# Kernel optimization log

Hardware: AMD Instinct MI355X
Metric: run time of the kernel (lower is better)

The kernel has to match this reference:

```python
import jax, jax.numpy as jnp
import numpy as np

B, IN, OUT, K, RES, WDIM = 8, 512, 512, 3, 64, 512
CONV_RC = 1.0 / np.sqrt(K * K * IN).astype(np.float32)   # gain*lrmul/sqrt(fan_in), gain=lrmul=1
DENSE_RC = 1.0 / np.sqrt(WDIM).astype(np.float32)
CONV_INIT_STD = float(CONV_RC)   # init_std = he_std / lrmul
DENSE_INIT_STD = float(DENSE_RC)


def setup_inputs() -> dict:
    key = jax.random.key(0)
    k1, k2, k3, k4 = jax.random.split(key, 4)
    return {
        "x": jax.random.normal(k1, (B, IN, RES, RES), jnp.float32),
        "y": jax.random.normal(k2, (B, WDIM), jnp.float32),
        "w": jax.random.normal(k3, (K, K, IN, OUT), jnp.float32) * CONV_INIT_STD,
        "w_mod": jax.random.normal(k4, (WDIM, IN), jnp.float32) * DENSE_INIT_STD,
        "b_mod": jnp.zeros((IN,), jnp.float32),
    }


def reference(x, y, w, w_mod, b_mod):
    # equalized-lr runtime scaling
    w_s = w * CONV_RC                                   # [K,K,IN,OUT]
    # style: s = dense(y) + bias + 1
    s = y @ (w_mod * DENSE_RC) + b_mod + 1.0            # [B,IN]
    # modulate per-sample weights
    ww = w_s[None] * s[:, None, None, :, None]          # [B,K,K,IN,OUT]
    # demodulate
    d = jax.lax.rsqrt(jnp.sum(jnp.square(ww), axis=(1, 2, 3)) + 1e-8)  # [B,OUT]
    ww = ww * d[:, None, None, None, :]
    # fused modconv: grouped conv with groups = B
    xr = x.reshape(1, B * IN, RES, RES)
    wk = jnp.transpose(ww, (1, 2, 3, 0, 4)).reshape(K, K, IN, B * OUT)
    out = jax.lax.conv_general_dilated(
        xr, wk, window_strides=(1, 1), padding="SAME",
        dimension_numbers=("NCHW", "HWIO", "NCHW"),
        feature_group_count=B)
    return out.reshape(B, OUT, RES, RES)
```

## Files before the change

kernel.cpp:

```cpp
#include <hip/hip_runtime.h>
#include <hip/hip_bf16.h>

typedef __bf16 bf16x8 __attribute__((ext_vector_type(8)));
typedef float f32x16 __attribute__((ext_vector_type(16)));
typedef unsigned short u16;
typedef u16 u16x8 __attribute__((ext_vector_type(8)));

#define DENSE_RC 0.0441941738f
#define CONV_RC  0.0147313913f

__device__ inline u16 f2bf(float v) {
  union { float f; unsigned u; } x; x.f = v;
  unsigned r = x.u + 0x7fffu + ((x.u >> 16) & 1u);
  return (u16)(r >> 16);
}

__device__ inline void gload16(const void* g, void* l) {
  __builtin_amdgcn_global_load_lds(
      (const __attribute__((address_space(1))) unsigned int*)g,
      (__attribute__((address_space(3))) unsigned int*)l, 16, 0, 0);
}

__global__ void style_k(const float* __restrict__ y, const float* __restrict__ wm,
                        const float* __restrict__ bm, float* __restrict__ s) {
  const int tid = threadIdx.x, lane = tid & 63, wv = tid >> 6;
  const int idx = blockIdx.x * 64 + lane;
  const int b = idx >> 9, i = idx & 511;
  const float* yb = y + b * 512;
  float acc = 0.f;
  const int j0 = wv * 128;
#pragma unroll 8
  for (int j = j0; j < j0 + 128; ++j) acc += yb[j] * wm[j * 512 + i];
  __shared__ float red[4][64];
  red[wv][lane] = acc;
  __syncthreads();
  if (wv == 0) {
    float a = red[0][lane] + red[1][lane] + red[2][lane] + red[3][lane];
    s[idx] = a * DENSE_RC + bm[i] + 1.0f;
  }
}

__global__ void wsq_k(const float* __restrict__ w, float* __restrict__ wsq) {
  const int idx = blockIdx.x * 256 + threadIdx.x;
  float a = 0.f;
#pragma unroll
  for (int t = 0; t < 9; ++t) { float v = w[(size_t)t * 262144 + idx]; a += v * v; }
  wsq[idx] = a;
}

__global__ void demod_k(const float* __restrict__ s, const float* __restrict__ wsq,
                        float* __restrict__ dmd) {
  const int tid = threadIdx.x, lane = tid & 63, wv = tid >> 6;
  const int idx = blockIdx.x * 64 + lane;
  const int b = idx >> 9, o = idx & 511;
  const float* sb = s + b * 512;
  float a = 0.f;
  const int i0 = wv * 128;
#pragma unroll 4
  for (int i = i0; i < i0 + 128; ++i) { float sv = sb[i]; a += sv * sv * wsq[i * 512 + o]; }
  __shared__ float red[4][64];
  red[wv][lane] = a;
  __syncthreads();
  if (wv == 0) {
    float t = red[0][lane] + red[1][lane] + red[2][lane] + red[3][lane];
    dmd[idx] = rsqrtf(t * (CONV_RC * CONV_RC) + 1e-8f);
  }
}

__global__ void modw_k(const float* __restrict__ w, const float* __restrict__ s,
                       const float* __restrict__ dmd, u16* __restrict__ wwb) {
  const int blk = blockIdx.x;
  const int ob = blk & 7, ib = (blk >> 3) & 15, t = blk >> 7;
  __shared__ float lw[32][65];
  const int tid = threadIdx.x;
#pragma unroll
  for (int k = 0; k < 8; ++k) {
    const int e = tid + k * 256;
    const int i = e >> 6, o = e & 63;
    lw[i][o] = w[(size_t)t * 262144 + (size_t)(ib * 32 + i) * 512 + ob * 64 + o];
  }
  __syncthreads();
  const int oo = tid >> 2, q = tid & 3;
  const int ii0 = q * 8;
  for (int b = 0; b < 8; ++b) {
    const float f = CONV_RC * dmd[b * 512 + ob * 64 + oo];
    u16x8 pk;
#pragma unroll
    for (int j = 0; j < 8; ++j)
      pk[j] = f2bf(lw[ii0 + j][oo] * s[b * 512 + ib * 32 + ii0 + j] * f);
    *(u16x8*)(wwb + ((size_t)(b * 9 + t) * 512 + ob * 64 + oo) * 512 + ib * 32 + ii0) = pk;
  }
}

__global__ void border_k(u16* __restrict__ xpad) {
  const int idx = blockIdx.x * 256 + threadIdx.x;
  const int chunk = idx & 63;
  const int p = (idx >> 6) % 260;
  const int b = idx / (260 * 64);
  int row, col;
  if (p < 66)       { row = 0;       col = p; }
  else if (p < 132) { row = 65;      col = p - 66; }
  else if (p < 196) { row = p - 131; col = 0; }
  else              { row = p - 195; col = 65; }
  u16x8 z = {0, 0, 0, 0, 0, 0, 0, 0};
  *(u16x8*)(xpad + ((size_t)(b * 66 + row) * 66 + col) * 512 + chunk * 8) = z;
}

__global__ void fill_k(const float* __restrict__ x, u16* __restrict__ xpad) {
  const int blk = blockIdx.x;
  const int ib = blk & 3, hh = (blk >> 2) & 63, b = blk >> 8;
  __shared__ float lx[128][65];
  const int tid = threadIdx.x;
#pragma unroll
  for (int k = 0; k < 2; ++k) {
    const int u = tid + k * 256;
    const int i = u >> 2, w0 = (u & 3) * 16;
    const float* src = x + (size_t)((b * 512 + ib * 128 + i) * 64 + hh) * 64 + w0;
    float tmp[16];
    ((float4*)tmp)[0] = ((const float4*)src)[0];
    ((float4*)tmp)[1] = ((const float4*)src)[1];
    ((float4*)tmp)[2] = ((const float4*)src)[2];
    ((float4*)tmp)[3] = ((const float4*)src)[3];
#pragma unroll
    for (int j = 0; j < 16; ++j) lx[i][w0 + j] = tmp[j];
  }
  __syncthreads();
  const int c = tid >> 2, q = tid & 3;
  const size_t base = ((size_t)(b * 66 + hh + 1) * 66 + (c + 1)) * 512 + ib * 128;
#pragma unroll
  for (int k = 0; k < 4; ++k) {
    const int irow = k * 32 + q * 8;
    u16x8 pk;
#pragma unroll
    for (int j = 0; j < 8; ++j) pk[j] = f2bf(lx[irow + j][c]);
    *(u16x8*)(xpad + base + irow) = pk;
  }
}

__global__ __launch_bounds__(256, 2) void conv_k(const u16* __restrict__ xpad,
                                                 const u16* __restrict__ wwb,
                                                 float* __restrict__ out) {
  __shared__ __align__(1024) char SM[79104];
  const int raw = (int)blockIdx.x;
  const int pt = raw >> 6, ot = (raw >> 3) & 7, b = raw & 7;
  const int tid = threadIdx.x;
  const int lane = tid & 63, wv = tid >> 6;
  const int h0 = pt * 8;

  const size_t xbase = (size_t)(b * 66 + h0) * (66 * 512);

  const u16* sp[10];
#pragma unroll
  for (int r = 0; r < 10; ++r) {
    const int cc = tid + r * 256;
    if (cc < 1152) {
      const int lc = cc ^ ((cc >> 3) & 3);
      const int t = lc >> 7, o = (lc >> 1) & 63, i8 = lc & 1;
      sp[r] = wwb + ((size_t)(b * 9 + t) * 512 + ot * 64 + o) * 512 + i8 * 8;
    } else {
      const int p = cc - 1152;
      const int lc = p ^ ((p >> 3) & 3);
      const int rc = lc >> 1, i8 = lc & 1;
      sp[r] = xpad + xbase + (size_t)rc * 512 + i8 * 8;
    }
  }

  const int l2 = ((lane & 31) << 1) | (lane >> 5);
  const int AoffT = (l2 ^ ((l2 >> 3) & 3)) * 16;
  int Boff[4][3];
#pragma unroll
  for (int rr = 0; rr < 4; ++rr)
#pragma unroll
    for (int tx = 0; tx < 3; ++tx) {
      const int ch = ((2 * wv + rr) * 66 + tx) * 2 + l2;
      Boff[rr][tx] = (ch ^ ((ch >> 3) & 3)) * 16;
    }

  f32x16 acc[2][2][2];
#pragma unroll
  for (int mi = 0; mi < 2; ++mi)
#pragma unroll
    for (int hf = 0; hf < 2; ++hf)
#pragma unroll
      for (int n = 0; n < 2; ++n)
#pragma unroll
        for (int e = 0; e < 16; ++e) acc[mi][hf][n][e] = 0.f;

#define LOADB(bf, rr, tx, ofs) { \
    const char* _p = SM + (ofs) + 18432 + Boff[rr][tx]; \
    bf[0] = *(const bf16x8*)_p; bf[1] = *(const bf16x8*)(_p + 1024); }
#define LOADA(af, t, ofs) { \
    const char* _p = SM + (ofs) + AoffT + (t) * 2048; \
    af[0] = *(const bf16x8*)_p; af[1] = *(const bf16x8*)(_p + 1024); }
#define TAP(af, Blo, Bhi) \
    __builtin_amdgcn_s_setprio(1); \
    acc[0][0][0] = __builtin_amdgcn_mfma_f32_32x32x16_bf16(af[0], Blo[0], acc[0][0][0], 0, 0, 0); \
    acc[0][0][1] = __builtin_amdgcn_mfma_f32_32x32x16_bf16(af[0], Blo[1], acc[0][0][1], 0, 0, 0); \
    acc[0][1][0] = __builtin_amdgcn_mfma_f32_32x32x16_bf16(af[0], Bhi[0], acc[0][1][0], 0, 0, 0); \
    acc[0][1][1] = __builtin_amdgcn_mfma_f32_32x32x16_bf16(af[0], Bhi[1], acc[0][1][1], 0, 0, 0); \
    acc[1][0][0] = __builtin_amdgcn_mfma_f32_32x32x16_bf16(af[1], Blo[0], acc[1][0][0], 0, 0, 0); \
    acc[1][0][1] = __builtin_amdgcn_mfma_f32_32x32x16_bf16(af[1], Blo[1], acc[1][0][1], 0, 0, 0); \
    acc[1][1][0] = __builtin_amdgcn_mfma_f32_32x32x16_bf16(af[1], Bhi[0], acc[1][1][0], 0, 0, 0); \
    acc[1][1][1] = __builtin_amdgcn_mfma_f32_32x32x16_bf16(af[1], Bhi[1], acc[1][1][1], 0, 0, 0); \
    __builtin_amdgcn_s_setprio(0);

  auto stage = [&](int ofs) {
#pragma unroll
    for (int r = 0; r < 9; ++r)
      gload16(sp[r], SM + ofs + (tid + r * 256) * 16);
    if (tid < 168) gload16(sp[9], SM + ofs + (tid + 2304) * 16);
#pragma unroll
    for (int r = 0; r < 10; ++r) sp[r] += 16;
  };

  auto compute = [&](int ofs) {
#pragma unroll
    for (int tx = 0; tx < 3; ++tx) {
      bf16x8 R0[2], R1[2], R2[2], R3[2], af0[2], af1[2], af2[2];
      LOADB(R0, 0, tx, ofs);
      LOADB(R1, 1, tx, ofs);
      LOADA(af0, tx, ofs);
      TAP(af0, R0, R1);
      LOADB(R2, 2, tx, ofs);
      LOADA(af1, 3 + tx, ofs);
      TAP(af1, R1, R2);
      LOADB(R3, 3, tx, ofs);
      LOADA(af2, 6 + tx, ofs);
      TAP(af2, R2, R3);
    }
  };

  stage(0);
  asm volatile("s_waitcnt vmcnt(0)" ::: "memory");
  __syncthreads();

  int cofs = 0, nofs = 39552;
  for (int kb = 0; kb < 31; ++kb) {
    stage(nofs);
    compute(cofs);
    asm volatile("s_waitcnt vmcnt(0)" ::: "memory");
    __syncthreads();
    const int tsw = cofs; cofs = nofs; nofs = tsw;
  }
  compute(cofs);

  const int pxl = lane & 31, oh = (lane >> 5) * 4;
#pragma unroll
  for (int mi = 0; mi < 2; ++mi)
#pragma unroll
    for (int hf = 0; hf < 2; ++hf) {
      const int h = h0 + 2 * wv + hf;
#pragma unroll
      for (int n = 0; n < 2; ++n) {
        const int wc = n * 32 + pxl;
#pragma unroll
        for (int reg = 0; reg < 16; ++reg) {
          const int o = ot * 64 + mi * 32 + (reg & 3) + 8 * (reg >> 2) + oh;
          out[((size_t)(b * 512 + o) * 64 + h) * 64 + wc] = acc[mi][hf][n][reg];
        }
      }
    }
#undef LOADB
#undef LOADA
#undef TAP
}

extern "C" void kernel_launch(void* const* d_in, const int* in_sizes, int n_in,
                              void* d_out, int out_size, void* d_ws, size_t ws_size,
                              hipStream_t stream) {
  const float* x     = (const float*)d_in[0];
  const float* y     = (const float*)d_in[1];
  const float* w     = (const float*)d_in[2];
  const float* w_mod = (const float*)d_in[3];
  const float* b_mod = (const float*)d_in[4];
  float* out = (float*)d_out;

  char* ws = (char*)d_ws;
  float* s    = (float*)(ws);
  float* dmd  = (float*)(ws + 16384);
  float* wsq  = (float*)(ws + 32768);
  u16*   wwb  = (u16*)(ws + 32768 + 1048576);
  u16*   xpad = (u16*)(ws + 32768 + 1048576 + 37748736);

  style_k<<<64, 256, 0, stream>>>(y, w_mod, b_mod, s);
  wsq_k<<<1024, 256, 0, stream>>>(w, wsq);
  demod_k<<<64, 256, 0, stream>>>(s, wsq, dmd);
  modw_k<<<1152, 256, 0, stream>>>(w, s, dmd, wwb);
  border_k<<<520, 256, 0, stream>>>(xpad);
  fill_k<<<2048, 256, 0, stream>>>(x, xpad);
  conv_k<<<512, 256, 0, stream>>>(xpad, wwb, out);
}
```

Measured before the change: 185.9 us.

## Use single-buffered 32-channel K tiles instead of double-buffered 16-channel stages

The conv main loop now stages 32 input channels per iteration into one LDS buffer of about 79KB, replacing two ~40KB buffers of 16 channels. That halves the iteration count and the barriers. Each iteration now loads, waits, computes and syncs with no overlap of global loads against MFMA work, and the setprio hints are gone. The LDS layout and swizzle are rewritten to match the wider tiles, so each tap now issues twice as many MFMAs.

```diff
diff --git a/kernel.cpp b/kernel.cpp
--- a/kernel.cpp
+++ b/kernel.cpp
@@ -149,30 +149,34 @@
 
   const size_t xbase = (size_t)(b * 66 + h0) * (66 * 512);
 
-  const u16* sp[10];
-#pragma unroll
-  for (int r = 0; r < 10; ++r) {
+  const u16* aw[9];
+  const u16* ax[11];
+#pragma unroll
+  for (int r = 0; r < 9; ++r) {
     const int cc = tid + r * 256;
-    if (cc < 1152) {
-      const int lc = cc ^ ((cc >> 3) & 3);
-      const int t = lc >> 7, o = (lc >> 1) & 63, i8 = lc & 1;
-      sp[r] = wwb + ((size_t)(b * 9 + t) * 512 + ot * 64 + o) * 512 + i8 * 8;
-    } else {
-      const int p = cc - 1152;
-      const int lc = p ^ ((p >> 3) & 3);
-      const int rc = lc >> 1, i8 = lc & 1;
-      sp[r] = xpad + xbase + (size_t)rc * 512 + i8 * 8;
-    }
-  }
-
-  const int l2 = ((lane & 31) << 1) | (lane >> 5);
-  const int AoffT = (l2 ^ ((l2 >> 3) & 3)) * 16;
+    const int lc = cc ^ ((cc >> 3) & 3);
+    const int i8 = lc & 3, o = (lc >> 2) & 63, t = lc >> 8;
+    aw[r] = wwb + ((size_t)(b * 9 + t) * 512 + ot * 64 + o) * 512 + i8 * 8;
+  }
+#pragma unroll
+  for (int r = 0; r < 11; ++r) {
+    const int c2 = tid + r * 256;
+    const int lc = c2 ^ ((c2 >> 3) & 3);
+    const int i8 = lc & 3, rc = lc >> 2;
+    ax[r] = xpad + xbase + (size_t)rc * 512 + i8 * 8;
+  }
+  const bool extra = (tid < 80);
+
+  const int pxl = lane & 31, i5 = lane >> 5;
+  const int cbA = pxl * 4 + i5;
+  const int AbO = (cbA ^ ((cbA >> 3) & 3)) * 16;
   int Boff[4][3];
 #pragma unroll
   for (int rr = 0; rr < 4; ++rr)
 #pragma unroll
     for (int tx = 0; tx < 3; ++tx) {
-      const int ch = ((2 * wv + rr) * 66 + tx) * 2 + l2;
+      const int m = (2 * wv + rr) * 66 + tx + pxl;
+      const int ch = m * 4 + i5;
       Boff[rr][tx] = (ch ^ ((ch >> 3) & 3)) * 16;
     }
 
@@ -186,65 +190,69 @@
 #pragma unroll
         for (int e = 0; e < 16; ++e) acc[mi][hf][n][e] = 0.f;
 
-#define LOADB(bf, rr, tx, ofs) { \
-    const char* _p = SM + (ofs) + 18432 + Boff[rr][tx]; \
-    bf[0] = *(const bf16x8*)_p; bf[1] = *(const bf16x8*)(_p + 1024); }
-#define LOADA(af, t, ofs) { \
-    const char* _p = SM + (ofs) + AoffT + (t) * 2048; \
-    af[0] = *(const bf16x8*)_p; af[1] = *(const bf16x8*)(_p + 1024); }
+#define LOADB(R, rr, tx) { \
+    const int _o = Boff[rr][tx]; \
+    R[0] = *(const bf16x8*)(SM + 36864 + _o); \
+    R[1] = *(const bf16x8*)(SM + 36864 + (_o ^ 32)); \
+    R[2] = *(const bf16x8*)(SM + 36864 + _o + 2048); \
+    R[3] = *(const bf16x8*)(SM + 36864 + ((_o + 2048) ^ 32)); }
+#define LOADA(af, t) { \
+    const int _a = AbO + (t) * 4096; \
+    af[0] = *(const bf16x8*)(SM + _a); \
+    af[1] = *(const bf16x8*)(SM + (_a ^ 32)); \
+    af[2] = *(const bf16x8*)(SM + _a + 2048); \
+    af[3] = *(const bf16x8*)(SM + ((_a + 2048) ^ 32)); }
 #define TAP(af, Blo, Bhi) \
-    __builtin_amdgcn_s_setprio(1); \
     acc[0][0][0] = __builtin_amdgcn_mfma_f32_32x32x16_bf16(af[0], Blo[0], acc[0][0][0], 0, 0, 0); \
-    acc[0][0][1] = __builtin_amdgcn_mfma_f32_32x32x16_bf16(af[0], Blo[1], acc[0][0][1], 0, 0, 0); \
+    acc[0][0][1] = __builtin_amdgcn_mfma_f32_32x32x16_bf16(af[0], Blo[2], acc[0][0][1], 0, 0, 0); \
     acc[0][1][0] = __builtin_amdgcn_mfma_f32_32x32x16_bf16(af[0], Bhi[0], acc[0][1][0], 0, 0, 0); \
-    acc[0][1][1] = __builtin_amdgcn_mfma_f32_32x32x16_bf16(af[0], Bhi[1], acc[0][1][1], 0, 0, 0); \
-    acc[1][0][0] = __builtin_amdgcn_mfma_f32_32x32x16_bf16(af[1], Blo[0], acc[1][0][0], 0, 0, 0); \
-    acc[1][0][1] = __builtin_amdgcn_mfma_f32_32x32x16_bf16(af[1], Blo[1], acc[1][0][1], 0, 0, 0); \
-    acc[1][1][0] = __builtin_amdgcn_mfma_f32_32x32x16_bf16(af[1], Bhi[0], acc[1][1][0], 0, 0, 0); \
-    acc[1][1][1] = __builtin_amdgcn_mfma_f32_32x32x16_bf16(af[1], Bhi[1], acc[1][1][1], 0, 0, 0); \
-    __builtin_amdgcn_s_setprio(0);
-
-  auto stage = [&](int ofs) {
+    acc[0][1][1] = __builtin_amdgcn_mfma_f32_32x32x16_bf16(af[0], Bhi[2], acc[0][1][1], 0, 0, 0); \
+    acc[1][0][0] = __builtin_amdgcn_mfma_f32_32x32x16_bf16(af[2], Blo[0], acc[1][0][0], 0, 0, 0); \
+    acc[1][0][1] = __builtin_amdgcn_mfma_f32_32x32x16_bf16(af[2], Blo[2], acc[1][0][1], 0, 0, 0); \
+    acc[1][1][0] = __builtin_amdgcn_mfma_f32_32x32x16_bf16(af[2], Bhi[0], acc[1][1][0], 0, 0, 0); \
+    acc[1][1][1] = __builtin_amdgcn_mfma_f32_32x32x16_bf16(af[2], Bhi[2], acc[1][1][1], 0, 0, 0); \
+    acc[0][0][0] = __builtin_amdgcn_mfma_f32_32x32x16_bf16(af[1], Blo[1], acc[0][0][0], 0, 0, 0); \
+    acc[0][0][1] = __builtin_amdgcn_mfma_f32_32x32x16_bf16(af[1], Blo[3], acc[0][0][1], 0, 0, 0); \
+    acc[0][1][0] = __builtin_amdgcn_mfma_f32_32x32x16_bf16(af[1], Bhi[1], acc[0][1][0], 0, 0, 0); \
+    acc[0][1][1] = __builtin_amdgcn_mfma_f32_32x32x16_bf16(af[1], Bhi[3], acc[0][1][1], 0, 0, 0); \
+    acc[1][0][0] = __builtin_amdgcn_mfma_f32_32x32x16_bf16(af[3], Blo[1], acc[1][0][0], 0, 0, 0); \
+    acc[1][0][1] = __builtin_amdgcn_mfma_f32_32x32x16_bf16(af[3], Blo[3], acc[1][0][1], 0, 0, 0); \
+    acc[1][1][0] = __builtin_amdgcn_mfma_f32_32x32x16_bf16(af[3], Bhi[1], acc[1][1][0], 0, 0, 0); \
+    acc[1][1][1] = __builtin_amdgcn_mfma_f32_32x32x16_bf16(af[3], Bhi[3], acc[1][1][1], 0, 0, 0);
+
+  for (int kb = 0; kb < 16; ++kb) {
 #pragma unroll
     for (int r = 0; r < 9; ++r)
-      gload16(sp[r], SM + ofs + (tid + r * 256) * 16);
-    if (tid < 168) gload16(sp[9], SM + ofs + (tid + 2304) * 16);
-#pragma unroll
-    for (int r = 0; r < 10; ++r) sp[r] += 16;
-  };
-
-  auto compute = [&](int ofs) {
+      gload16(aw[r], SM + (tid + r * 256) * 16);
+#pragma unroll
+    for (int r = 0; r < 10; ++r)
+      gload16(ax[r], SM + 36864 + (tid + r * 256) * 16);
+    if (extra) gload16(ax[10], SM + 36864 + (tid + 2560) * 16);
+#pragma unroll
+    for (int r = 0; r < 9; ++r) aw[r] += 32;
+#pragma unroll
+    for (int r = 0; r < 11; ++r) ax[r] += 32;
+    asm volatile("s_waitcnt vmcnt(0)" ::: "memory");
+    __syncthreads();
+
 #pragma unroll
     for (int tx = 0; tx < 3; ++tx) {
-      bf16x8 R0[2], R1[2], R2[2], R3[2], af0[2], af1[2], af2[2];
-      LOADB(R0, 0, tx, ofs);
-      LOADB(R1, 1, tx, ofs);
-      LOADA(af0, tx, ofs);
+      bf16x8 R0[4], R1[4], R2[4], R3[4], af0[4], af1[4], af2[4];
+      LOADB(R0, 0, tx);
+      LOADB(R1, 1, tx);
+      LOADA(af0, tx);
       TAP(af0, R0, R1);
-      LOADB(R2, 2, tx, ofs);
-      LOADA(af1, 3 + tx, ofs);
+      LOADB(R2, 2, tx);
+      LOADA(af1, 3 + tx);
       TAP(af1, R1, R2);
-      LOADB(R3, 3, tx, ofs);
-      LOADA(af2, 6 + tx, ofs);
+      LOADB(R3, 3, tx);
+      LOADA(af2, 6 + tx);
       TAP(af2, R2, R3);
     }
-  };
-
-  stage(0);
-  asm volatile("s_waitcnt vmcnt(0)" ::: "memory");
-  __syncthreads();
-
-  int cofs = 0, nofs = 39552;
-  for (int kb = 0; kb < 31; ++kb) {
-    stage(nofs);
-    compute(cofs);
-    asm volatile("s_waitcnt vmcnt(0)" ::: "memory");
     __syncthreads();
-    const int tsw = cofs; cofs = nofs; nofs = tsw;
-  }
-  compute(cofs);
-
-  const int pxl = lane & 31, oh = (lane >> 5) * 4;
+  }
+
+  const int o4 = i5 * 4;
 #pragma unroll
   for (int mi = 0; mi < 2; ++mi)
 #pragma unroll
@@ -255,7 +263,7 @@
         const int wc = n * 32 + pxl;
 #pragma unroll
         for (int reg = 0; reg < 16; ++reg) {
-          const int o = ot * 64 + mi * 32 + (reg & 3) + 8 * (reg >> 2) + oh;
+          const int o = ot * 64 + mi * 32 + (reg & 3) + 8 * (reg >> 2) + o4;
           out[((size_t)(b * 512 + o) * 64 + h) * 64 + wc] = acc[mi][hf][n][reg];
         }
       }
```

Result: faster. 174.0 us (-6.4%).
